# Performance work log

Measured on AMD Instinct MI355X. Metric: run time of the kernel, lower is better.

The kernel has to match this reference:

```python
import jax, jax.numpy as jnp
import numpy as np

LUT_DIM = 33  # standard 33^3 color LUT


def setup_inputs() -> dict:
    key = jax.random.key(0)
    k1, k2 = jax.random.split(key)
    # learned 3D LUT: [out_channels=3, D_b, D_g, D_r]
    lut = jax.random.normal(k1, (3, LUT_DIM, LUT_DIM, LUT_DIM), dtype=jnp.float32) * 0.1
    # input image batch in [0, 1): [B, 3, H, W]
    x = jax.random.uniform(k2, (4, 3, 1024, 1024), dtype=jnp.float32)
    return {"lut": lut, "x": x}


def reference(lut, x):
    """Trilinear interpolation of a 3D color LUT (image-adaptive-3DLUT forward).

    lut: [3, D, D, D] laid out as lut[c, ib, ig, ir] (flat index ir + ig*D + ib*D*D)
    x:   [B, 3, H, W] with channels (r, g, b) in [0, 1]
    returns: [B, 3, H, W]
    """
    dim = lut.shape[-1]
    scale = dim - 1  # 1 / binsize

    r, g, b = x[:, 0], x[:, 1], x[:, 2]  # each [B, H, W]

    def cell(c):
        s = c * scale
        idx = jnp.clip(jnp.floor(s), 0, scale - 1).astype(jnp.int32)
        return idx, s - idx.astype(s.dtype)  # integer cell, fractional offset

    ir, dr = cell(r)
    ig, dg = cell(g)
    ib, db = cell(b)

    lut_flat = lut.reshape(3, -1)  # [3, D^3], tiny and cache-resident

    out = jnp.zeros((3,) + r.shape, dtype=x.dtype)  # [3, B, H, W]
    # 8 corners of the enclosing LUT cell, trilinear weights
    for or_ in (0, 1):
        wr = dr if or_ else (1.0 - dr)
        for og in (0, 1):
            wg = dg if og else (1.0 - dg)
            for ob in (0, 1):
                wb = db if ob else (1.0 - db)
                flat = ((ib + ob) * dim + (ig + og)) * dim + (ir + or_)  # [B, H, W]
                corner = lut_flat[:, flat]  # gather -> [3, B, H, W]
                out = out + (wr * wg * wb)[None] * corner

    return jnp.transpose(out, (1, 0, 2, 3))  # [B, 3, H, W]
```

## Files before the change

kernel.cpp:

```cpp
#include <hip/hip_runtime.h>
#include <hip/hip_fp16.h>


#define LUT_D      33
#define LUT_DD     (LUT_D * LUT_D)
#define LUT_N      (LUT_D * LUT_D * LUT_D)
#define HW4        (1024 * 1024 / 4)
#define NGROUPS    (4 * HW4)
#define NCHUNKS    256
#define THREADS    1024
#define ITERS      (NGROUPS / NCHUNKS / THREADS)
#define PACK_ROUNDS ((LUT_N + THREADS - 1) / THREADS)

typedef float vfloat4 __attribute__((ext_vector_type(4)));

__device__ __forceinline__ unsigned int pack2(float a, float b) {
    union { __half2 h; unsigned int u; } cv;
    cv.h = __floats2half2_rn(a, b);
    return cv.u;
}
__device__ __forceinline__ float2 unpack2(unsigned int p) {
    union { unsigned int u; __half2 h; } cv;
    cv.u = p;
    return __half22float2(cv.h);
}

__global__ __launch_bounds__(THREADS)
void lut3d_trilerp_kernel(const float* __restrict__ lut,
                          const float* __restrict__ x,
                          float* __restrict__ out) {
    extern __shared__ __align__(16) unsigned int W[];

    const int t     = (int)threadIdx.x;
    const int chunk = blockIdx.x;

    const float4* x4 = (const float4*)x;
    float4*       o4 = (float4*)out;
    const int g0 = chunk * (NGROUPS / NCHUNKS) + t;

    int   ibase[ITERS];
    int   idx[ITERS][4];
    float dr[ITERS][4], dg[ITERS][4], db[ITERS][4];
#pragma unroll
    for (int it = 0; it < ITERS; ++it) {
        const int g     = g0 + it * THREADS;
        const int b_img = g >> 18;
        const int hw4   = g & (HW4 - 1);
        ibase[it] = b_img * 3 * HW4 + hw4;
        const float4 R = x4[ibase[it]];
        const float4 G = x4[ibase[it] + HW4];
        const float4 B = x4[ibase[it] + 2 * HW4];
        const float rr[4] = {R.x, R.y, R.z, R.w};
        const float gg[4] = {G.x, G.y, G.z, G.w};
        const float bb[4] = {B.x, B.y, B.z, B.w};
#pragma unroll
        for (int k = 0; k < 4; ++k) {
            const float sr = rr[k] * 32.0f;
            const float sg = gg[k] * 32.0f;
            const float sb = bb[k] * 32.0f;
            const float fr = fminf(fmaxf(floorf(sr), 0.0f), 31.0f);
            const float fg = fminf(fmaxf(floorf(sg), 0.0f), 31.0f);
            const float fb = fminf(fmaxf(floorf(sb), 0.0f), 31.0f);
            dr[it][k] = sr - fr;
            dg[it][k] = sg - fg;
            db[it][k] = sb - fb;
            idx[it][k] = ((int)fb * LUT_D + (int)fg) * LUT_D + (int)fr;
        }
    }

    for (int c = 0; c < 3; ++c) {
        if (c) __syncthreads();

        const float* Lc = lut + c * LUT_N;
#pragma unroll 4
        for (int r = 0; r < PACK_ROUNDS; ++r) {
            const int i = r * THREADS + t;
            if (i < LUT_N) {
                const float a = Lc[i];
                const float b = (i + 1 < LUT_N) ? Lc[i + 1] : 0.0f;
                W[i] = pack2(a, b);
            }
        }
        __syncthreads();

#pragma unroll
        for (int it = 0; it < ITERS; ++it) {
            unsigned int qA[4], qB[4], qC[4], qD[4];
#pragma unroll
            for (int k = 0; k < 4; ++k) {
                const int i0 = idx[it][k];
                qA[k] = W[i0];
                qB[k] = W[i0 + LUT_D];
                qC[k] = W[i0 + LUT_DD];
                qD[k] = W[i0 + LUT_DD + LUT_D];
            }
            float oo[4];
#pragma unroll
            for (int k = 0; k < 4; ++k) {
                const float2 a00 = unpack2(qA[k]);
                const float2 a01 = unpack2(qB[k]);
                const float2 a10 = unpack2(qC[k]);
                const float2 a11 = unpack2(qD[k]);
                const float l00 = a00.x + dr[it][k] * (a00.y - a00.x);
                const float l01 = a01.x + dr[it][k] * (a01.y - a01.x);
                const float l10 = a10.x + dr[it][k] * (a10.y - a10.x);
                const float l11 = a11.x + dr[it][k] * (a11.y - a11.x);
                const float l0  = l00 + dg[it][k] * (l01 - l00);
                const float l1  = l10 + dg[it][k] * (l11 - l10);
                oo[k] = l0 + db[it][k] * (l1 - l0);
            }
            vfloat4 v = {oo[0], oo[1], oo[2], oo[3]};
            __builtin_nontemporal_store(v, (vfloat4*)&o4[ibase[it] + c * HW4]);
        }
    }
}

extern "C" void kernel_launch(void* const* d_in, const int* in_sizes, int n_in,
                              void* d_out, int out_size, void* d_ws, size_t ws_size,
                              hipStream_t stream) {
    const float* lut = (const float*)d_in[0];
    const float* x   = (const float*)d_in[1];
    float*       out = (float*)d_out;
    (void)d_ws; (void)ws_size;

    const size_t lds_bytes = (size_t)LUT_N * 4;
    lut3d_trilerp_kernel<<<NCHUNKS, THREADS, lds_bytes, stream>>>(lut, x, out);
}
```

Before: 128.1 us.

## Prepack half2 LUT in separate kernel and stage to LDS via direct global-load-LDS

A small pre-kernel packs each LUT channel into half2 neighbour pairs in workspace, padded to a 16-byte-aligned stride. The main kernel then copies each channel into LDS with 16-byte global_load_lds DMA-style loads instead of per-block scalar load+convert+store. The first channel's copy is issued after the pixel loads so the two overlap. This removes the per-block packing arithmetic and scalar LDS writes repeated across 256 blocks, at the cost of an extra kernel launch and a workspace round trip.

```diff
diff --git a/kernel.cpp b/kernel.cpp
--- a/kernel.cpp
+++ b/kernel.cpp
@@ -2,15 +2,16 @@
 #include <hip/hip_fp16.h>
 
 
-#define LUT_D      33
-#define LUT_DD     (LUT_D * LUT_D)
-#define LUT_N      (LUT_D * LUT_D * LUT_D)
-#define HW4        (1024 * 1024 / 4)
-#define NGROUPS    (4 * HW4)
-#define NCHUNKS    256
-#define THREADS    1024
-#define ITERS      (NGROUPS / NCHUNKS / THREADS)
-#define PACK_ROUNDS ((LUT_N + THREADS - 1) / THREADS)
+#define LUT_D     33
+#define LUT_DD    (LUT_D * LUT_D)
+#define LUT_N     (LUT_D * LUT_D * LUT_D)
+#define CH_STRIDE 35940
+#define STAGE_G   (CH_STRIDE / 4)
+#define HW4       (1024 * 1024 / 4)
+#define NGROUPS   (4 * HW4)
+#define NCHUNKS   256
+#define THREADS   1024
+#define ITERS     (NGROUPS / NCHUNKS / THREADS)
 
 typedef float vfloat4 __attribute__((ext_vector_type(4)));
 
@@ -25,8 +26,19 @@
     return __half22float2(cv.h);
 }
 
+__global__ __launch_bounds__(256)
+void lut_pack_kernel(const float* __restrict__ lut, unsigned int* __restrict__ W) {
+    const int t = blockIdx.x * 256 + (int)threadIdx.x;
+    if (t >= 3 * LUT_N) return;
+    const int c = t / LUT_N;
+    const int i = t - c * LUT_N;
+    const float a = lut[t];
+    const float b = (i + 1 < LUT_N) ? lut[t + 1] : 0.0f;
+    W[c * CH_STRIDE + i] = pack2(a, b);
+}
+
 __global__ __launch_bounds__(THREADS)
-void lut3d_trilerp_kernel(const float* __restrict__ lut,
+void lut3d_trilerp_kernel(const unsigned int* __restrict__ Wsrc,
                           const float* __restrict__ x,
                           float* __restrict__ out) {
     extern __shared__ __align__(16) unsigned int W[];
@@ -38,21 +50,37 @@
     float4*       o4 = (float4*)out;
     const int g0 = chunk * (NGROUPS / NCHUNKS) + t;
 
-    int   ibase[ITERS];
-    int   idx[ITERS][4];
-    float dr[ITERS][4], dg[ITERS][4], db[ITERS][4];
+    float4 R[ITERS], G[ITERS], B[ITERS];
+    int ibase[ITERS];
 #pragma unroll
     for (int it = 0; it < ITERS; ++it) {
         const int g     = g0 + it * THREADS;
         const int b_img = g >> 18;
         const int hw4   = g & (HW4 - 1);
         ibase[it] = b_img * 3 * HW4 + hw4;
-        const float4 R = x4[ibase[it]];
-        const float4 G = x4[ibase[it] + HW4];
-        const float4 B = x4[ibase[it] + 2 * HW4];
-        const float rr[4] = {R.x, R.y, R.z, R.w};
-        const float gg[4] = {G.x, G.y, G.z, G.w};
-        const float bb[4] = {B.x, B.y, B.z, B.w};
+        R[it] = x4[ibase[it]];
+        G[it] = x4[ibase[it] + HW4];
+        B[it] = x4[ibase[it] + 2 * HW4];
+    }
+
+#pragma unroll
+    for (int s = 0; s < 9; ++s) {
+        const int gid = s * THREADS + t;
+        if (gid < STAGE_G) {
+            __builtin_amdgcn_global_load_lds(
+                (const __attribute__((address_space(1))) void*)(Wsrc + gid * 4),
+                (__attribute__((address_space(3))) void*)(W + gid * 4),
+                16, 0, 0);
+        }
+    }
+
+    int   idx[ITERS][4];
+    float dr[ITERS][4], dg[ITERS][4], db[ITERS][4];
+#pragma unroll
+    for (int it = 0; it < ITERS; ++it) {
+        const float rr[4] = {R[it].x, R[it].y, R[it].z, R[it].w};
+        const float gg[4] = {G[it].x, G[it].y, G[it].z, G[it].w};
+        const float bb[4] = {B[it].x, B[it].y, B[it].z, B[it].w};
 #pragma unroll
         for (int k = 0; k < 4; ++k) {
             const float sr = rr[k] * 32.0f;
@@ -68,21 +96,10 @@
         }
     }
 
+    __syncthreads();
+
+#pragma unroll
     for (int c = 0; c < 3; ++c) {
-        if (c) __syncthreads();
-
-        const float* Lc = lut + c * LUT_N;
-#pragma unroll 4
-        for (int r = 0; r < PACK_ROUNDS; ++r) {
-            const int i = r * THREADS + t;
-            if (i < LUT_N) {
-                const float a = Lc[i];
-                const float b = (i + 1 < LUT_N) ? Lc[i + 1] : 0.0f;
-                W[i] = pack2(a, b);
-            }
-        }
-        __syncthreads();
-
 #pragma unroll
         for (int it = 0; it < ITERS; ++it) {
             unsigned int qA[4], qB[4], qC[4], qD[4];
@@ -112,17 +129,36 @@
             vfloat4 v = {oo[0], oo[1], oo[2], oo[3]};
             __builtin_nontemporal_store(v, (vfloat4*)&o4[ibase[it] + c * HW4]);
         }
+
+        if (c < 2) {
+            __syncthreads();
+            const unsigned int* src = Wsrc + (c + 1) * CH_STRIDE;
+#pragma unroll
+            for (int s = 0; s < 9; ++s) {
+                const int gid = s * THREADS + t;
+                if (gid < STAGE_G) {
+                    __builtin_amdgcn_global_load_lds(
+                        (const __attribute__((address_space(1))) void*)(src + gid * 4),
+                        (__attribute__((address_space(3))) void*)(W + gid * 4),
+                        16, 0, 0);
+                }
+            }
+            __syncthreads();
+        }
     }
 }
 
 extern "C" void kernel_launch(void* const* d_in, const int* in_sizes, int n_in,
                               void* d_out, int out_size, void* d_ws, size_t ws_size,
                               hipStream_t stream) {
-    const float* lut = (const float*)d_in[0];
-    const float* x   = (const float*)d_in[1];
-    float*       out = (float*)d_out;
-    (void)d_ws; (void)ws_size;
+    const float*  lut = (const float*)d_in[0];
+    const float*  x   = (const float*)d_in[1];
+    float*        out = (float*)d_out;
+    unsigned int* W   = (unsigned int*)d_ws;
 
-    const size_t lds_bytes = (size_t)LUT_N * 4;
-    lut3d_trilerp_kernel<<<NCHUNKS, THREADS, lds_bytes, stream>>>(lut, x, out);
+    const int pack_grid = (3 * LUT_N + 255) / 256;
+    lut_pack_kernel<<<pack_grid, 256, 0, stream>>>(lut, W);
+
+    const size_t lds_bytes = (size_t)CH_STRIDE * 4;
+    lut3d_trilerp_kernel<<<NCHUNKS, THREADS, lds_bytes, stream>>>(W, x, out);
 }
```

Result: faster. 111.8 us (median of 2 runs) (-12.7%).
